# Performance work log

Measured on AMD Instinct MI355X. Metric: run time of the kernel, lower is better.

Reference implementation:

```python
import jax, jax.numpy as jnp
import numpy as np

N, E, F_IN, H1, H2, C = 100000, 800000, 182, 128, 64, 2


def setup_inputs() -> dict:
    key = jax.random.key(0)
    ks = jax.random.split(key, 10)
    s = 0.05
    return {
        "x": jax.random.normal(ks[0], (N, F_IN), dtype=jnp.float32),
        "edge_index": jax.random.randint(ks[1], (2, E), 0, N, dtype=jnp.int32),
        "W1_l": jax.random.normal(ks[2], (H1, F_IN), dtype=jnp.float32) * s,
        "W1_r": jax.random.normal(ks[3], (H1, F_IN), dtype=jnp.float32) * s,
        "b1": jnp.zeros((H1,), dtype=jnp.float32),
        "W2_l": jax.random.normal(ks[4], (H2, H1), dtype=jnp.float32) * s,
        "W2_r": jax.random.normal(ks[5], (H2, H1), dtype=jnp.float32) * s,
        "b2": jnp.zeros((H2,), dtype=jnp.float32),
        "W_lin": jax.random.normal(ks[6], (C, H2), dtype=jnp.float32) * s,
        "b_lin": jnp.zeros((C,), dtype=jnp.float32),
    }


def _sage_conv(x, src, dst, Wl, Wr, b):
    # mean-aggregate neighbor messages x[src] onto dst, then two linears
    msg = x[src]                                            # [E, F]
    ssum = jax.ops.segment_sum(msg, dst, num_segments=N)    # [N, F]
    cnt = jax.ops.segment_sum(jnp.ones((src.shape[0], 1), x.dtype), dst, num_segments=N)
    mean = ssum / jnp.maximum(cnt, 1.0)                     # [N, F]
    return mean @ Wl.T + x @ Wr.T + b                       # [N, F_out]


def reference(x, edge_index, W1_l, W1_r, b1, W2_l, W2_r, b2, W_lin, b_lin):
    src, dst = edge_index[0], edge_index[1]
    h = jax.nn.relu(_sage_conv(x, src, dst, W1_l, W1_r, b1))   # dropout is identity in eval
    h = jax.nn.relu(_sage_conv(h, src, dst, W2_l, W2_r, b2))
    logits = h @ W_lin.T + b_lin
    return jax.nn.log_softmax(logits, axis=1)
```

## Files before the change

kernel.cpp:

```cpp
#include <hip/hip_runtime.h>
#include <hip/hip_bf16.h>
#include <math.h>

#define F_IN 182
#define H1   128
#define H2   64

typedef short bf16x8 __attribute__((ext_vector_type(8)));
typedef float f32x4 __attribute__((ext_vector_type(4)));

__device__ __forceinline__ float b2f(short s) {
    unsigned u = ((unsigned)(unsigned short)s) << 16;
    return __builtin_bit_cast(float, u);
}
__device__ __forceinline__ short f2b(float f) {
    return __builtin_bit_cast(short, __float2bfloat16(f));
}
__device__ __forceinline__ short2 f2x2(float2 f) {
    short2 r;
    r.x = f2b(f.x);
    r.y = f2b(f.y);
    return r;
}

#define GLOAD16(g, l) __builtin_amdgcn_global_load_lds( \
    (const __attribute__((address_space(1))) void*)(g), \
    (__attribute__((address_space(3))) void*)(l), 16, 0, 0)

__global__ __launch_bounds__(256) void prelude(
    int* __restrict__ cnt, int Nn, int zB,
    const float* __restrict__ W1l, const float* __restrict__ W1r, short* __restrict__ wc1,
    const float* __restrict__ W2l, const float* __restrict__ W2r, short* __restrict__ wc2)
{
    int b = blockIdx.x, tid = threadIdx.x;
    if (b < zB) {
        int i = (b * 256 + tid) * 4;
        if (i + 4 <= Nn) {
            int4 z = make_int4(0, 0, 0, 0);
            *(int4*)(cnt + i) = z;
        } else {
            for (int j = i; j < Nn; ++j) cnt[j] = 0;
        }
        return;
    }
    b -= zB;
    if (b < 192) {
        int idx = b * 256 + tid;
        int r = idx / 192, k = idx - r * 192;
        float v = 0.f;
        if (k < F_IN) v = (r < 128) ? W1l[r * F_IN + k] : W1r[(r - 128) * F_IN + k];
        wc1[idx] = f2b(v);
        return;
    }
    b -= 192;
    {
        int idx = b * 256 + tid;
        int r = idx >> 7, k = idx & 127;
        float v = (r < 64) ? W2l[r * 128 + k] : W2r[(r - 64) * 128 + k];
        wc2[idx] = f2b(v);
    }
}

__global__ __launch_bounds__(256) void scan_block(const int* __restrict__ in,
                                                  int* __restrict__ out,
                                                  int* __restrict__ bsums, int Nn) {
    __shared__ int s[256];
    int b = blockIdx.x, t = threadIdx.x;
    int base = b * 2048 + t * 8;
    int v[8]; int sum = 0;
#pragma unroll
    for (int i = 0; i < 8; ++i) { int idx = base + i; v[i] = (idx < Nn) ? in[idx] : 0; sum += v[i]; }
    s[t] = sum; __syncthreads();
    for (int off = 1; off < 256; off <<= 1) {
        int x = (t >= off) ? s[t - off] : 0; __syncthreads();
        s[t] += x; __syncthreads();
    }
    int excl = s[t] - sum;
    if (t == 255) bsums[b] = s[255];
    int run = excl;
#pragma unroll
    for (int i = 0; i < 8; ++i) { int idx = base + i; if (idx < Nn) out[idx] = run; run += v[i]; }
}

__global__ __launch_bounds__(256) void scan_add(int* __restrict__ offs,
                                                const int* __restrict__ bsums,
                                                int nb, int Nn) {
    __shared__ int sbs[64];
    int t = threadIdx.x;
    if (t < 64) {
        int v = (t < nb) ? bsums[t] : 0;
        int s = v;
#pragma unroll
        for (int off = 1; off < 64; off <<= 1) {
            int u = __shfl_up(s, off, 64);
            if (t >= off) s += u;
        }
        sbs[t] = s - v;
    }
    __syncthreads();
    int i = blockIdx.x * 256 + t;
    if (i < Nn) offs[i] += sbs[i >> 11];
}

__global__ __launch_bounds__(256) void csr_scatter(const int* __restrict__ srcv,
                                                   const int* __restrict__ dstv,
                                                   const int* __restrict__ rank,
                                                   const int* __restrict__ offs,
                                                   int* __restrict__ csr, int E) {
    int base = (blockIdx.x * 256 + threadIdx.x) * 4;
    if (base + 4 <= E) {
        int4 d = *(const int4*)(dstv + base);
        int4 s = *(const int4*)(srcv + base);
        int4 rk = *(const int4*)(rank + base);
        csr[offs[d.x] + rk.x] = s.x;
        csr[offs[d.y] + rk.y] = s.y;
        csr[offs[d.z] + rk.z] = s.z;
        csr[offs[d.w] + rk.w] = s.w;
    } else {
        for (int e = base; e < E; ++e) csr[offs[dstv[e]] + rank[e]] = srcv[e];
    }
}

template <int NC, int KK, int KREAL, bool AF32, bool DEG>
__global__ __launch_bounds__(512) void gemm_fused(
    const void* __restrict__ Ap, const short* __restrict__ Wcat,
    short* __restrict__ outL, short* __restrict__ outR, int M,
    const int* __restrict__ dstv, int* __restrict__ cnt, int* __restrict__ rank,
    int E, int degB)
{
    constexpr int BM = 128, BK = 64;
    constexpr int WN = NC / 4;
    constexpr int NJ = WN / 16;
    constexpr int CB = NC * 8 / 512;
    __shared__ __attribute__((aligned(16))) short sA[BM * BK];
    __shared__ __attribute__((aligned(16))) short sB[NC * BK];
    int tid = threadIdx.x;

    if (DEG && (int)blockIdx.x < degB) {
        int base = ((int)blockIdx.x * 512 + tid) * 4;
        if (base + 4 <= E) {
            int4 d = *(const int4*)(dstv + base);
            int4 rk;
            rk.x = atomicAdd(&cnt[d.x], 1);
            rk.y = atomicAdd(&cnt[d.y], 1);
            rk.z = atomicAdd(&cnt[d.z], 1);
            rk.w = atomicAdd(&cnt[d.w], 1);
            *(int4*)(rank + base) = rk;
        } else {
            for (int e = base; e < E; ++e) rank[e] = atomicAdd(&cnt[dstv[e]], 1);
        }
        return;
    }
    int bx = DEG ? ((int)blockIdx.x - degB) : (int)blockIdx.x;
    int wid = tid >> 6, lane = tid & 63;
    int wr = wid >> 2, wc = wid & 3;
    int row0 = bx * BM;
    bool full = (row0 + BM <= M);
    f32x4 acc[4][NJ] = {};
#pragma unroll
    for (int ksi = 0; ksi < KK / BK; ++ksi) {
        const int k0 = ksi * BK;
        if (AF32) {
            const float* Af = (const float*)Ap;
#pragma unroll
            for (int it = 0; it < 2; ++it) {
                int i = it * 512 + tid;
                int r = i >> 3, oct = i & 7;
                int gr = row0 + r;
                int gk = k0 + oct * 8;
                bf16x8 v = {};
                if (gr < M) {
                    const float* p = Af + (size_t)gr * KREAL + gk;
                    if (k0 + BK <= KREAL) {
                        float2 f0 = *(const float2*)(p + 0);
                        float2 f1 = *(const float2*)(p + 2);
                        float2 f2 = *(const float2*)(p + 4);
                        float2 f3 = *(const float2*)(p + 6);
                        short2 p0 = f2x2(f0), p1 = f2x2(f1), p2 = f2x2(f2), p3 = f2x2(f3);
                        v[0] = p0.x; v[1] = p0.y; v[2] = p1.x; v[3] = p1.y;
                        v[4] = p2.x; v[5] = p2.y; v[6] = p3.x; v[7] = p3.y;
                    } else {
#pragma unroll
                        for (int j = 0; j < 4; ++j) {
                            if (gk + 2 * j + 2 <= KREAL) {
                                short2 pj = f2x2(*(const float2*)(p + 2 * j));
                                v[2 * j] = pj.x; v[2 * j + 1] = pj.y;
                            }
                        }
                    }
                }
                *(bf16x8*)((char*)sA + r * 128 + ((oct * 16) ^ ((r & 7) << 4))) = v;
            }
        } else {
            const char* Ab = (const char*)Ap;
            if (full) {
#pragma unroll
                for (int c = 0; c < 2; ++c) {
                    int idx = (wid * 2 + c) * 64 + lane;
                    int r = idx >> 3, cs = (idx & 7) * 16;
                    const char* g = Ab + (size_t)(row0 + r) * (KK * 2) + k0 * 2 + (cs ^ ((r & 7) << 4));
                    GLOAD16(g, (char*)sA + (size_t)(wid * 2 + c) * 1024);
                }
            } else {
                for (int t = tid; t < BM * 8; t += 512) {
                    int r = t >> 3, kc = (t & 7) * 16;
                    bf16x8 v = {};
                    int gr = row0 + r;
                    if (gr < M) v = *(const bf16x8*)(Ab + (size_t)gr * (KK * 2) + k0 * 2 + kc);
                    *(bf16x8*)((char*)sA + r * 128 + (kc ^ ((r & 7) << 4))) = v;
                }
            }
        }
#pragma unroll
        for (int c = 0; c < CB; ++c) {
            int idx = (wid * CB + c) * 64 + lane;
            int r = idx >> 3, cs = (idx & 7) * 16;
            const char* g = (const char*)Wcat + (size_t)r * (KK * 2) + k0 * 2 + (cs ^ ((r & 7) << 4));
            GLOAD16(g, (char*)sB + (size_t)(wid * CB + c) * 1024);
        }
        __syncthreads();
        int rl = lane & 15;
        int sw = (rl & 7) << 4;
#pragma unroll
        for (int ks = 0; ks < 2; ++ks) {
            int kb2 = ks * 64 + (lane >> 4) * 16;
            int cswz = kb2 ^ sw;
            bf16x8 af[4];
#pragma unroll
            for (int mi = 0; mi < 4; ++mi) {
                int row = wr * 64 + mi * 16 + rl;
                af[mi] = *(const bf16x8*)((const char*)sA + row * 128 + cswz);
            }
#pragma unroll
            for (int ni = 0; ni < NJ; ++ni) {
                int rowb = wc * WN + ni * 16 + rl;
                bf16x8 bfr = *(const bf16x8*)((const char*)sB + rowb * 128 + cswz);
#pragma unroll
                for (int mi = 0; mi < 4; ++mi)
                    acc[mi][ni] = __builtin_amdgcn_mfma_f32_16x16x32_bf16(af[mi], bfr, acc[mi][ni], 0, 0, 0);
            }
        }
        __syncthreads();
    }
    constexpr int HN = NC / 2;
#pragma unroll
    for (int mi = 0; mi < 4; ++mi) {
#pragma unroll
        for (int ni = 0; ni < NJ; ++ni) {
            int gc = wc * WN + ni * 16 + (lane & 15);
#pragma unroll
            for (int r = 0; r < 4; ++r) {
                int gr = row0 + wr * 64 + mi * 16 + (lane >> 4) * 4 + r;
                if (gr < M) {
                    short v = f2b(acc[mi][ni][r]);
                    if (gc < HN) outL[(size_t)gr * HN + gc] = v;
                    else         outR[(size_t)gr * HN + gc - HN] = v;
                }
            }
        }
    }
}

__global__ __launch_bounds__(256) void agg_fuse1(const int* __restrict__ offs,
                                                 const int* __restrict__ degs,
                                                 const int* __restrict__ csr,
                                                 const short* __restrict__ yl,
                                                 const short* __restrict__ yr,
                                                 const float* __restrict__ bias,
                                                 short* __restrict__ h, int Nn) {
    int gid = blockIdx.x * 16 + (threadIdx.x >> 4);
    int l = threadIdx.x & 15;
    if (gid >= Nn) return;
    int start = offs[gid], deg = degs[gid];
    const int co = l * 8;
    float a[8] = {};
    int t = 0;
    for (; t + 8 <= deg; t += 8) {
        int idx[8];
#pragma unroll
        for (int q = 0; q < 8; ++q) idx[q] = csr[start + t + q];
        bf16x8 vv[8];
#pragma unroll
        for (int q = 0; q < 8; ++q) vv[q] = *(const bf16x8*)(yl + (size_t)idx[q] * H1 + co);
#pragma unroll
        for (int j = 0; j < 8; ++j) {
            float s = 0.f;
#pragma unroll
            for (int q = 0; q < 8; ++q) s += b2f(vv[q][j]);
            a[j] += s;
        }
    }
    for (; t + 4 <= deg; t += 4) {
        int i0 = csr[start + t], i1 = csr[start + t + 1];
        int i2 = csr[start + t + 2], i3 = csr[start + t + 3];
        bf16x8 v0 = *(const bf16x8*)(yl + (size_t)i0 * H1 + co);
        bf16x8 v1 = *(const bf16x8*)(yl + (size_t)i1 * H1 + co);
        bf16x8 v2 = *(const bf16x8*)(yl + (size_t)i2 * H1 + co);
        bf16x8 v3 = *(const bf16x8*)(yl + (size_t)i3 * H1 + co);
#pragma unroll
        for (int j = 0; j < 8; ++j)
            a[j] += b2f(v0[j]) + b2f(v1[j]) + b2f(v2[j]) + b2f(v3[j]);
    }
    for (; t < deg; ++t) {
        int s = csr[start + t];
        bf16x8 v = *(const bf16x8*)(yl + (size_t)s * H1 + co);
#pragma unroll
        for (int j = 0; j < 8; ++j) a[j] += b2f(v[j]);
    }
    float inv = 1.f / fmaxf((float)deg, 1.f);
    bf16x8 rv = *(const bf16x8*)(yr + (size_t)gid * H1 + co);
    bf16x8 o;
#pragma unroll
    for (int j = 0; j < 4; ++j) {
        float r0 = fmaxf(a[2 * j] * inv + b2f(rv[2 * j]) + bias[co + 2 * j], 0.f);
        float r1 = fmaxf(a[2 * j + 1] * inv + b2f(rv[2 * j + 1]) + bias[co + 2 * j + 1], 0.f);
        o[2 * j] = f2b(r0); o[2 * j + 1] = f2b(r1);
    }
    *(bf16x8*)(h + (size_t)gid * H1 + co) = o;
}

__global__ __launch_bounds__(256) void agg_head2(const int* __restrict__ offs,
                                                 const int* __restrict__ degs,
                                                 const int* __restrict__ csr,
                                                 const short* __restrict__ yl,
                                                 const short* __restrict__ yr,
                                                 const float* __restrict__ bias,
                                                 const float* __restrict__ Wlin,
                                                 const float* __restrict__ blin,
                                                 float* __restrict__ out, int Nn) {
    int gid = blockIdx.x * 16 + (threadIdx.x >> 4);
    int l = threadIdx.x & 15;
    if (gid >= Nn) return;
    int start = offs[gid], deg = degs[gid];
    const int co = l * 4;
    float a[4] = {};
    int t = 0;
    for (; t + 8 <= deg; t += 8) {
        int idx[8];
#pragma unroll
        for (int q = 0; q < 8; ++q) idx[q] = csr[start + t + q];
        short4 vv[8];
#pragma unroll
        for (int q = 0; q < 8; ++q) vv[q] = *(const short4*)(yl + (size_t)idx[q] * H2 + co);
#pragma unroll
        for (int q = 0; q < 8; ++q) {
            a[0] += b2f(vv[q].x); a[1] += b2f(vv[q].y);
            a[2] += b2f(vv[q].z); a[3] += b2f(vv[q].w);
        }
    }
    for (; t + 4 <= deg; t += 4) {
        int i0 = csr[start + t], i1 = csr[start + t + 1];
        int i2 = csr[start + t + 2], i3 = csr[start + t + 3];
        short4 v0 = *(const short4*)(yl + (size_t)i0 * H2 + co);
        short4 v1 = *(const short4*)(yl + (size_t)i1 * H2 + co);
        short4 v2 = *(const short4*)(yl + (size_t)i2 * H2 + co);
        short4 v3 = *(const short4*)(yl + (size_t)i3 * H2 + co);
        a[0] += b2f(v0.x) + b2f(v1.x) + b2f(v2.x) + b2f(v3.x);
        a[1] += b2f(v0.y) + b2f(v1.y) + b2f(v2.y) + b2f(v3.y);
        a[2] += b2f(v0.z) + b2f(v1.z) + b2f(v2.z) + b2f(v3.z);
        a[3] += b2f(v0.w) + b2f(v1.w) + b2f(v2.w) + b2f(v3.w);
    }
    for (; t < deg; ++t) {
        int s = csr[start + t];
        short4 v = *(const short4*)(yl + (size_t)s * H2 + co);
        a[0] += b2f(v.x); a[1] += b2f(v.y); a[2] += b2f(v.z); a[3] += b2f(v.w);
    }
    float inv = 1.f / fmaxf((float)deg, 1.f);
    short4 rv = *(const short4*)(yr + (size_t)gid * H2 + co);
    float h0 = fmaxf(a[0] * inv + b2f(rv.x) + bias[co + 0], 0.f);
    float h1v = fmaxf(a[1] * inv + b2f(rv.y) + bias[co + 1], 0.f);
    float h2v = fmaxf(a[2] * inv + b2f(rv.z) + bias[co + 2], 0.f);
    float h3v = fmaxf(a[3] * inv + b2f(rv.w) + bias[co + 3], 0.f);
    float g0 = h0 * Wlin[co] + h1v * Wlin[co + 1] + h2v * Wlin[co + 2] + h3v * Wlin[co + 3];
    float g1 = h0 * Wlin[64 + co] + h1v * Wlin[64 + co + 1] + h2v * Wlin[64 + co + 2] + h3v * Wlin[64 + co + 3];
#pragma unroll
    for (int m = 8; m >= 1; m >>= 1) {
        g0 += __shfl_xor(g0, m, 16);
        g1 += __shfl_xor(g1, m, 16);
    }
    if (l == 0) {
        g0 += blin[0]; g1 += blin[1];
        float mx = fmaxf(g0, g1);
        float lse = mx + logf(expf(g0 - mx) + expf(g1 - mx));
        float2 r; r.x = g0 - lse; r.y = g1 - lse;
        ((float2*)out)[gid] = r;
    }
}

extern "C" void kernel_launch(void* const* d_in, const int* in_sizes, int n_in,
                              void* d_out, int out_size, void* d_ws, size_t ws_size,
                              hipStream_t stream) {
    const float* x    = (const float*)d_in[0];
    const int*   ei   = (const int*)d_in[1];
    const float* W1l  = (const float*)d_in[2];
    const float* W1r  = (const float*)d_in[3];
    const float* b1   = (const float*)d_in[4];
    const float* W2l  = (const float*)d_in[5];
    const float* W2r  = (const float*)d_in[6];
    const float* b2   = (const float*)d_in[7];
    const float* Wlin = (const float*)d_in[8];
    const float* blin = (const float*)d_in[9];
    float* outp = (float*)d_out;

    const int N = in_sizes[0] / F_IN;
    const int E = in_sizes[1] / 2;
    const int* srcv = ei;
    const int* dstv = ei + E;

    char* ws = (char*)d_ws;
    size_t o = 0;
    auto alloc = [&](size_t bytes) { size_t r = o; o += (bytes + 255) & ~(size_t)255; return r; };
    int* cnt_i  = (int*)(ws + alloc((size_t)N * 4));
    int* offs   = (int*)(ws + alloc((size_t)N * 4));
    int* bsums  = (int*)(ws + alloc(1024));
    int* rank   = (int*)(ws + alloc((size_t)E * 4));
    int* csr    = (int*)(ws + alloc((size_t)E * 4));
    short* wc1  = (short*)(ws + alloc((size_t)256 * 192 * 2));
    short* wc2  = (short*)(ws + alloc((size_t)128 * 128 * 2));
    short* y1l  = (short*)(ws + alloc((size_t)N * H1 * 2));
    short* y1r  = (short*)(ws + alloc((size_t)N * H1 * 2));
    short* h1   = (short*)(ws + alloc((size_t)N * H1 * 2));
    short* y2l  = y1l;
    short* y2r  = y1r;

    const int zB   = (N + 1023) / 1024;
    const int degB = (E + 2047) / 2048;
    const int nb   = (N + 2047) / 2048;
    const int nthr = (N + 255) / 256;
    const int gblk = (N + 127) / 128;
    const int e4   = (E + 1023) / 1024;
    const int a16  = (N + 15) / 16;

    prelude<<<zB + 192 + 64, 256, 0, stream>>>(cnt_i, N, zB, W1l, W1r, wc1, W2l, W2r, wc2);

    gemm_fused<256, 192, F_IN, true, true><<<degB + gblk, 512, 0, stream>>>(
        x, wc1, y1l, y1r, N, dstv, cnt_i, rank, E, degB);

    scan_block<<<nb, 256, 0, stream>>>(cnt_i, offs, bsums, N);
    scan_add<<<nthr, 256, 0, stream>>>(offs, bsums, nb, N);

    csr_scatter<<<e4, 256, 0, stream>>>(srcv, dstv, rank, offs, csr, E);

    agg_fuse1<<<a16, 256, 0, stream>>>(offs, cnt_i, csr, y1l, y1r, b1, h1, N);

    gemm_fused<128, 128, 128, false, false><<<gblk, 512, 0, stream>>>(
        h1, wc2, y2l, y2r, N, nullptr, nullptr, nullptr, 0, 0);

    agg_head2<<<a16, 256, 0, stream>>>(offs, cnt_i, csr, y2l, y2r, b2, Wlin, blin, outp, N);
}
```

Before: 169.6 us.

## Fuse layer-1 aggregation with layer-2 GEMM and widen CSR scatter

Merges the layer-1 neighbour mean aggregation and ReLU with the layer-2 dual-linear GEMM in one kernel. Aggregated rows go straight into LDS as the GEMM A tile, so the h1 intermediate is never written to or read back from global memory. This removes one launch and an N×128 bf16 round trip. In exchange, each 512-thread block of about 64 KB LDS now does irregular gathers, which may lower occupancy and reduce latency hiding. The CSR scatter also handles 8 edges per thread instead of 4.

```diff
diff --git a/kernel.cpp b/kernel.cpp
--- a/kernel.cpp
+++ b/kernel.cpp
@@ -107,21 +107,28 @@
                                                    const int* __restrict__ rank,
                                                    const int* __restrict__ offs,
                                                    int* __restrict__ csr, int E) {
-    int base = (blockIdx.x * 256 + threadIdx.x) * 4;
-    if (base + 4 <= E) {
-        int4 d = *(const int4*)(dstv + base);
-        int4 s = *(const int4*)(srcv + base);
-        int4 rk = *(const int4*)(rank + base);
-        csr[offs[d.x] + rk.x] = s.x;
-        csr[offs[d.y] + rk.y] = s.y;
-        csr[offs[d.z] + rk.z] = s.z;
-        csr[offs[d.w] + rk.w] = s.w;
+    int base = (blockIdx.x * 256 + threadIdx.x) * 8;
+    if (base + 8 <= E) {
+        int4 d0 = *(const int4*)(dstv + base);
+        int4 d1 = *(const int4*)(dstv + base + 4);
+        int4 s0 = *(const int4*)(srcv + base);
+        int4 s1 = *(const int4*)(srcv + base + 4);
+        int4 r0 = *(const int4*)(rank + base);
+        int4 r1 = *(const int4*)(rank + base + 4);
+        csr[offs[d0.x] + r0.x] = s0.x;
+        csr[offs[d0.y] + r0.y] = s0.y;
+        csr[offs[d0.z] + r0.z] = s0.z;
+        csr[offs[d0.w] + r0.w] = s0.w;
+        csr[offs[d1.x] + r1.x] = s1.x;
+        csr[offs[d1.y] + r1.y] = s1.y;
+        csr[offs[d1.z] + r1.z] = s1.z;
+        csr[offs[d1.w] + r1.w] = s1.w;
     } else {
         for (int e = base; e < E; ++e) csr[offs[dstv[e]] + rank[e]] = srcv[e];
     }
 }
 
-template <int NC, int KK, int KREAL, bool AF32, bool DEG>
+template <int NC, int KK, int KREAL, bool DEG>
 __global__ __launch_bounds__(512) void gemm_fused(
     const void* __restrict__ Ap, const short* __restrict__ Wcat,
     short* __restrict__ outL, short* __restrict__ outR, int M,
@@ -155,12 +162,11 @@
     int wid = tid >> 6, lane = tid & 63;
     int wr = wid >> 2, wc = wid & 3;
     int row0 = bx * BM;
-    bool full = (row0 + BM <= M);
     f32x4 acc[4][NJ] = {};
 #pragma unroll
     for (int ksi = 0; ksi < KK / BK; ++ksi) {
         const int k0 = ksi * BK;
-        if (AF32) {
+        {
             const float* Af = (const float*)Ap;
 #pragma unroll
             for (int it = 0; it < 2; ++it) {
@@ -191,25 +197,6 @@
                 }
                 *(bf16x8*)((char*)sA + r * 128 + ((oct * 16) ^ ((r & 7) << 4))) = v;
             }
-        } else {
-            const char* Ab = (const char*)Ap;
-            if (full) {
-#pragma unroll
-                for (int c = 0; c < 2; ++c) {
-                    int idx = (wid * 2 + c) * 64 + lane;
-                    int r = idx >> 3, cs = (idx & 7) * 16;
-                    const char* g = Ab + (size_t)(row0 + r) * (KK * 2) + k0 * 2 + (cs ^ ((r & 7) << 4));
-                    GLOAD16(g, (char*)sA + (size_t)(wid * 2 + c) * 1024);
-                }
-            } else {
-                for (int t = tid; t < BM * 8; t += 512) {
-                    int r = t >> 3, kc = (t & 7) * 16;
-                    bf16x8 v = {};
-                    int gr = row0 + r;
-                    if (gr < M) v = *(const bf16x8*)(Ab + (size_t)gr * (KK * 2) + k0 * 2 + kc);
-                    *(bf16x8*)((char*)sA + r * 128 + (kc ^ ((r & 7) << 4))) = v;
-                }
-            }
         }
 #pragma unroll
         for (int c = 0; c < CB; ++c) {
@@ -261,62 +248,128 @@
     }
 }
 
-__global__ __launch_bounds__(256) void agg_fuse1(const int* __restrict__ offs,
-                                                 const int* __restrict__ degs,
-                                                 const int* __restrict__ csr,
-                                                 const short* __restrict__ yl,
-                                                 const short* __restrict__ yr,
-                                                 const float* __restrict__ bias,
-                                                 short* __restrict__ h, int Nn) {
-    int gid = blockIdx.x * 16 + (threadIdx.x >> 4);
-    int l = threadIdx.x & 15;
-    if (gid >= Nn) return;
-    int start = offs[gid], deg = degs[gid];
+__global__ __launch_bounds__(512) void agg_gemm2(
+    const int* __restrict__ offs, const int* __restrict__ degs, const int* __restrict__ csr,
+    const short* __restrict__ y1l, const short* __restrict__ y1r,
+    const float* __restrict__ b1, const short* __restrict__ wc2,
+    short* __restrict__ outL, short* __restrict__ outR, int M)
+{
+    constexpr int BM = 128, KK = 128, NC = 128;
+    constexpr int WN = NC / 4;
+    constexpr int NJ = WN / 16;
+    __shared__ __attribute__((aligned(16))) short sA[BM * KK];
+    __shared__ __attribute__((aligned(16))) short sB[NC * KK];
+    int tid = threadIdx.x;
+    int wid = tid >> 6, lane = tid & 63;
+    int wr = wid >> 2, wc = wid & 3;
+    int row0 = (int)blockIdx.x * BM;
+
+#pragma unroll
+    for (int it = 0; it < 4; ++it) {
+        int idx = (wid * 4 + it) * 64 + lane;
+        int r = idx >> 4, c16 = (idx & 15) * 16;
+        const char* g = (const char*)wc2 + (size_t)r * 256 + (c16 ^ ((r & 7) << 4));
+        GLOAD16(g, (char*)sB + (size_t)(wid * 4 + it) * 1024);
+    }
+
+    int rlocal = tid >> 4;
+    int l = tid & 15;
     const int co = l * 8;
-    float a[8] = {};
-    int t = 0;
-    for (; t + 8 <= deg; t += 8) {
-        int idx[8];
-#pragma unroll
-        for (int q = 0; q < 8; ++q) idx[q] = csr[start + t + q];
-        bf16x8 vv[8];
-#pragma unroll
-        for (int q = 0; q < 8; ++q) vv[q] = *(const bf16x8*)(yl + (size_t)idx[q] * H1 + co);
-#pragma unroll
-        for (int j = 0; j < 8; ++j) {
-            float s = 0.f;
-#pragma unroll
-            for (int q = 0; q < 8; ++q) s += b2f(vv[q][j]);
-            a[j] += s;
-        }
-    }
-    for (; t + 4 <= deg; t += 4) {
-        int i0 = csr[start + t], i1 = csr[start + t + 1];
-        int i2 = csr[start + t + 2], i3 = csr[start + t + 3];
-        bf16x8 v0 = *(const bf16x8*)(yl + (size_t)i0 * H1 + co);
-        bf16x8 v1 = *(const bf16x8*)(yl + (size_t)i1 * H1 + co);
-        bf16x8 v2 = *(const bf16x8*)(yl + (size_t)i2 * H1 + co);
-        bf16x8 v3 = *(const bf16x8*)(yl + (size_t)i3 * H1 + co);
-#pragma unroll
-        for (int j = 0; j < 8; ++j)
-            a[j] += b2f(v0[j]) + b2f(v1[j]) + b2f(v2[j]) + b2f(v3[j]);
-    }
-    for (; t < deg; ++t) {
-        int s = csr[start + t];
-        bf16x8 v = *(const bf16x8*)(yl + (size_t)s * H1 + co);
-#pragma unroll
-        for (int j = 0; j < 8; ++j) a[j] += b2f(v[j]);
-    }
-    float inv = 1.f / fmaxf((float)deg, 1.f);
-    bf16x8 rv = *(const bf16x8*)(yr + (size_t)gid * H1 + co);
-    bf16x8 o;
-#pragma unroll
-    for (int j = 0; j < 4; ++j) {
-        float r0 = fmaxf(a[2 * j] * inv + b2f(rv[2 * j]) + bias[co + 2 * j], 0.f);
-        float r1 = fmaxf(a[2 * j + 1] * inv + b2f(rv[2 * j + 1]) + bias[co + 2 * j + 1], 0.f);
-        o[2 * j] = f2b(r0); o[2 * j + 1] = f2b(r1);
-    }
-    *(bf16x8*)(h + (size_t)gid * H1 + co) = o;
+#pragma unroll
+    for (int rr = 0; rr < 4; ++rr) {
+        int r = rr * 32 + rlocal;
+        int gid = row0 + r;
+        bf16x8 o = {};
+        if (gid < M) {
+            int start = offs[gid], deg = degs[gid];
+            float a[8] = {};
+            int t = 0;
+            for (; t + 8 <= deg; t += 8) {
+                int idx[8];
+#pragma unroll
+                for (int q = 0; q < 8; ++q) idx[q] = csr[start + t + q];
+                bf16x8 vv[8];
+#pragma unroll
+                for (int q = 0; q < 8; ++q) vv[q] = *(const bf16x8*)(y1l + (size_t)idx[q] * H1 + co);
+#pragma unroll
+                for (int j = 0; j < 8; ++j) {
+                    float s = 0.f;
+#pragma unroll
+                    for (int q = 0; q < 8; ++q) s += b2f(vv[q][j]);
+                    a[j] += s;
+                }
+            }
+            for (; t + 4 <= deg; t += 4) {
+                int i0 = csr[start + t], i1 = csr[start + t + 1];
+                int i2 = csr[start + t + 2], i3 = csr[start + t + 3];
+                bf16x8 v0 = *(const bf16x8*)(y1l + (size_t)i0 * H1 + co);
+                bf16x8 v1 = *(const bf16x8*)(y1l + (size_t)i1 * H1 + co);
+                bf16x8 v2 = *(const bf16x8*)(y1l + (size_t)i2 * H1 + co);
+                bf16x8 v3 = *(const bf16x8*)(y1l + (size_t)i3 * H1 + co);
+#pragma unroll
+                for (int j = 0; j < 8; ++j)
+                    a[j] += b2f(v0[j]) + b2f(v1[j]) + b2f(v2[j]) + b2f(v3[j]);
+            }
+            for (; t < deg; ++t) {
+                int s = csr[start + t];
+                bf16x8 v = *(const bf16x8*)(y1l + (size_t)s * H1 + co);
+#pragma unroll
+                for (int j = 0; j < 8; ++j) a[j] += b2f(v[j]);
+            }
+            float inv = 1.f / fmaxf((float)deg, 1.f);
+            bf16x8 rv = *(const bf16x8*)(y1r + (size_t)gid * H1 + co);
+#pragma unroll
+            for (int j = 0; j < 8; ++j)
+                o[j] = f2b(fmaxf(a[j] * inv + b2f(rv[j]) + b1[co + j], 0.f));
+        }
+        *(bf16x8*)((char*)sA + r * 256 + ((co * 2) ^ ((r & 7) << 4))) = o;
+    }
+    __syncthreads();
+
+    f32x4 acc[4][NJ] = {};
+    int rl = lane & 15;
+    int sw = (rl & 7) << 4;
+#pragma unroll
+    for (int ks = 0; ks < 8; ++ks) {
+        int kb2 = ks * 16 + 0;
+        int kcol = ((ks & 3) * 4 + (lane >> 4)) * 16;
+        (void)kb2;
+        if (ks < 4) kcol = (ks * 4 + (lane >> 4)) * 16;
+        else        kcol = ((ks - 4) * 4 + (lane >> 4)) * 16;
+        if (ks >= 4) break;
+        int cswz = kcol ^ sw;
+        bf16x8 af[4];
+#pragma unroll
+        for (int mi = 0; mi < 4; ++mi) {
+            int row = wr * 64 + mi * 16 + rl;
+            af[mi] = *(const bf16x8*)((const char*)sA + row * 256 + cswz);
+        }
+#pragma unroll
+        for (int ni = 0; ni < NJ; ++ni) {
+            int rowb = wc * WN + ni * 16 + rl;
+            bf16x8 bfr = *(const bf16x8*)((const char*)sB + rowb * 256 + cswz);
+#pragma unroll
+            for (int mi = 0; mi < 4; ++mi)
+                acc[mi][ni] = __builtin_amdgcn_mfma_f32_16x16x32_bf16(af[mi], bfr, acc[mi][ni], 0, 0, 0);
+        }
+    }
+    constexpr int HN = NC / 2;
+#pragma unroll
+    for (int mi = 0; mi < 4; ++mi) {
+#pragma unroll
+        for (int ni = 0; ni < NJ; ++ni) {
+            int gc = wc * WN + ni * 16 + (lane & 15);
+#pragma unroll
+            for (int r = 0; r < 4; ++r) {
+                int gr = row0 + wr * 64 + mi * 16 + (lane >> 4) * 4 + r;
+                if (gr < M) {
+                    short v = f2b(acc[mi][ni][r]);
+                    if (gc < HN) outL[(size_t)gr * HN + gc] = v;
+                    else         outR[(size_t)gr * HN + gc - HN] = v;
+                }
+            }
+        }
+    }
 }
 
 __global__ __launch_bounds__(256) void agg_head2(const int* __restrict__ offs,
@@ -419,32 +472,28 @@
     short* wc2  = (short*)(ws + alloc((size_t)128 * 128 * 2));
     short* y1l  = (short*)(ws + alloc((size_t)N * H1 * 2));
     short* y1r  = (short*)(ws + alloc((size_t)N * H1 * 2));
-    short* h1   = (short*)(ws + alloc((size_t)N * H1 * 2));
-    short* y2l  = y1l;
-    short* y2r  = y1r;
+    short* y2l  = (short*)(ws + alloc((size_t)N * H2 * 2));
+    short* y2r  = (short*)(ws + alloc((size_t)N * H2 * 2));
 
     const int zB   = (N + 1023) / 1024;
     const int degB = (E + 2047) / 2048;
     const int nb   = (N + 2047) / 2048;
     const int nthr = (N + 255) / 256;
     const int gblk = (N + 127) / 128;
-    const int e4   = (E + 1023) / 1024;
+    const int e8   = (E + 2047) / 2048;
     const int a16  = (N + 15) / 16;
 
     prelude<<<zB + 192 + 64, 256, 0, stream>>>(cnt_i, N, zB, W1l, W1r, wc1, W2l, W2r, wc2);
 
-    gemm_fused<256, 192, F_IN, true, true><<<degB + gblk, 512, 0, stream>>>(
+    gemm_fused<256, 192, F_IN, true><<<degB + gblk, 512, 0, stream>>>(
         x, wc1, y1l, y1r, N, dstv, cnt_i, rank, E, degB);
 
     scan_block<<<nb, 256, 0, stream>>>(cnt_i, offs, bsums, N);
     scan_add<<<nthr, 256, 0, stream>>>(offs, bsums, nb, N);
 
-    csr_scatter<<<e4, 256, 0, stream>>>(srcv, dstv, rank, offs, csr, E);
-
-    agg_fuse1<<<a16, 256, 0, stream>>>(offs, cnt_i, csr, y1l, y1r, b1, h1, N);
-
-    gemm_fused<128, 128, 128, false, false><<<gblk, 512, 0, stream>>>(
-        h1, wc2, y2l, y2r, N, nullptr, nullptr, nullptr, 0, 0);
+    csr_scatter<<<e8, 256, 0, stream>>>(srcv, dstv, rank, offs, csr, E);
+
+    agg_gemm2<<<gblk, 512, 0, stream>>>(offs, cnt_i, csr, y1l, y1r, b1, wc2, y2l, y2r, N);
 
     agg_head2<<<a16, 256, 0, stream>>>(offs, cnt_i, csr, y2l, y2r, b2, Wlin, blin, outp, N);
 }
```

Measured after the change: 168.6 us. Within noise of the previous version (-0.6%).
